# Kernel optimization log

Measured on AMD Instinct MI355X. Metric: run time of the kernel, lower is better.

The kernel has to match this reference:

```python
import jax, jax.numpy as jnp
import numpy as np

# Dimensions: S=Scount nodes, R=Rcount(=n_classes), B=len(source_index)
S, R, IN_F, OUT_F, H, B, C = 10000, 16, 128, 128, 4, 2048, 16
NEG = -9e15


def _bn(x, g, b):
    # BatchNorm1d, training-mode batch statistics (biased var), eps=1e-5
    m = x.mean(0)
    v = x.var(0)
    return (x - m) / jnp.sqrt(v + 1e-5) * g + b


def setup_inputs() -> dict:
    key = jax.random.key(0)
    ks = jax.random.split(key, 13)
    n = lambda k, s: jax.random.normal(k, s, jnp.float32) * 0.1
    return {
        "inter_adj": jax.random.randint(ks[0], (S, R), 0, 2, jnp.int32),
        "city_adj": jax.random.randint(ks[1], (S, S), 0, 2, jnp.int32),
        "province_adj": jax.random.randint(ks[2], (S, S), 0, 2, jnp.int32),
        "source_index": jax.random.randint(ks[3], (B,), 0, S, jnp.int32),
        "Sfeat": n(ks[4], (S, IN_F)),
        "Rfeat": n(ks[5], (R, IN_F)),
        "W1": n(ks[6], (H, IN_F, OUT_F)),
        "W2": n(ks[7], (H, IN_F, OUT_F)),
        "a": n(ks[8], (H, 2 * OUT_F)),
        "a3": n(ks[9], (H, 2 * OUT_F)),
        "a4": n(ks[10], (H, 2 * OUT_F)),
        "bn1_g": jnp.ones((H, OUT_F), jnp.float32),
        "bn1_b": jnp.zeros((H, OUT_F), jnp.float32),
        "bn2_g": jnp.ones((H, OUT_F), jnp.float32),
        "bn2_b": jnp.zeros((H, OUT_F), jnp.float32),
        "outW": n(ks[11], (H * R, C)),
        "outA": n(ks[12], (2 * C,)),
    }


def _forward(inter_adj, city_adj, province_adj, src, Sfeat, Rfeat,
             W1, W2, a, a3, a4, bn1_g, bn1_b, bn2_g, bn2_b, outW, outA):
    Fd = OUT_F
    inter_m = inter_adj > 0            # [S, R]
    city_m = city_adj[src] > 0         # [B, S]
    prov_m = province_adj[src] > 0     # [B, S]
    # Dropout is identity (eval mode); the concat+matmul attention scores are
    # computed as separable rank-1 terms instead of materializing O(S*R*2F).

    def head(W1h, W2h, ah, a3h, a4h, g1h, b1h, g2h, b2h):
        h1 = Rfeat @ W1h               # [R, F]
        h2 = Sfeat @ W2h               # [S, F]
        h2s = h2[src]                  # [B, F]
        # e12[i,j] = lrelu(a[:F].h1[j] + a[F:].h2[i])
        e12 = jax.nn.leaky_relu((h2 @ ah[Fd:])[:, None] + (h1 @ ah[:Fd])[None, :], 0.2)
        att_i = jax.nn.softmax(jnp.where(inter_m, e12, NEG), axis=1)   # [S, R]
        # cat([h3, h3]) -> score constant over the neighbor axis
        e3 = jax.nn.leaky_relu(h2s @ (a3h[:Fd] + a3h[Fd:]), 0.2)[:, None]  # [B,1]
        att3 = jax.nn.softmax(jnp.where(city_m, e3, NEG), axis=1)      # [B, S]
        e4 = jax.nn.leaky_relu(h2s @ (a4h[:Fd] + a4h[Fd:]), 0.2)[:, None]
        att4 = jax.nn.softmax(jnp.where(prov_m, e4, NEG), axis=1)
        InterRC = att_i @ h1                        # [S, F]
        IntraNC = (att3 + att4).T @ h2s             # [S, F]
        v = jax.nn.leaky_relu(_bn(att_i.T @ h2, g1h, b1h), 0.2)  # [R, F]
        u = jax.nn.leaky_relu(_bn(InterRC + IntraNC, g2h, b2h), 0.2)  # [S, F]
        return jax.nn.elu(u @ v.T)                  # [S, R]

    hx = jax.vmap(head)(W1, W2, a, a3, a4, bn1_g, bn1_b, bn2_g, bn2_b)  # [H,S,R]
    x = jnp.transpose(hx, (1, 0, 2)).reshape(S, H * R)
    # output GraphAttentionLayer
    h = x @ outW                                    # [S, C]
    e = jax.nn.leaky_relu(h @ (outA[:C] + outA[C:]), 0.2)[:, None]  # [S,1]
    att = jax.nn.softmax(jnp.where(inter_m, jnp.broadcast_to(e, inter_m.shape), NEG), axis=1)
    # elu inside layer, then elu again in ablation2, then log_softmax
    return jax.nn.log_softmax(jax.nn.elu(jax.nn.elu(att * h)), axis=1)


def reference(inter_adj, city_adj, province_adj, source_index, Sfeat, Rfeat,
              W1, W2, a, a3, a4, bn1_g, bn1_b, bn2_g, bn2_b, outW, outA):
    return _forward(inter_adj, city_adj, province_adj, source_index, Sfeat, Rfeat,
                    W1, W2, a, a3, a4, bn1_g, bn1_b, bn2_g, bn2_b, outW, outA)
```

## Files before the change

### kernel.cpp

```cpp
#include <hip/hip_runtime.h>
#include <hip/hip_bf16.h>
#include <stdint.h>

#define S_N 10000
#define MPAD 10112
#define B_N 2048
#define F_N 128

typedef __bf16 bf16x8 __attribute__((ext_vector_type(8)));
typedef __bf16 bf16x4 __attribute__((ext_vector_type(4)));
typedef float  f32x4  __attribute__((ext_vector_type(4)));
typedef unsigned long long u64;
typedef unsigned int u32;
typedef unsigned short u16;

union Bh8 { __bf16 h[8]; bf16x8 v; };

__device__ __forceinline__ float lrelu02(float x) { return x >= 0.0f ? x : 0.2f * x; }
__device__ __forceinline__ float eluf(float x)    { return x > 0.0f ? x : expm1f(x); }

__global__ __launch_bounds__(256) void k_bits_pre(const int* __restrict__ adj_c,
        const int* __restrict__ adj_p, const int* __restrict__ src,
        const float* __restrict__ Sfeat, const float* __restrict__ Rfeat,
        const float* __restrict__ W1, const float* __restrict__ W2, const float* __restrict__ a,
        u64* __restrict__ tcity, u64* __restrict__ tprov,
        u32* __restrict__ cc, u32* __restrict__ pc,
        __bf16* __restrict__ SfB, __bf16* __restrict__ W2T, __bf16* __restrict__ h1T,
        float* __restrict__ q) {
    const int bid = blockIdx.x, t = threadIdx.x;
    if (bid < 1280) {
        const int sc = bid % 20, wb = (bid / 20) % 32, mat = bid / 640;
        const int l = t & 63, w = t >> 6;
        const int* adj = mat ? adj_p : adj_c;
        u64* tb = mat ? tprov : tcity;
        u32* cnt = mat ? pc : cc;
        __shared__ u64 wt[64][8];
        __shared__ u32 lc[64];
        if (t < 64) lc[t] = 0;
        __syncthreads();
        const int s1 = sc * 512 + t;
        const int s2 = s1 + 256;
        for (int bb = 0; bb < 64; ++bb) {
            int row = src[wb * 64 + bb];
            const int* rp = adj + (size_t)row * S_N;
            int v1 = (s1 < S_N) ? rp[s1] : 0;
            int v2 = (s2 < S_N) ? rp[s2] : 0;
            u64 b1 = __ballot(v1 > 0);
            u64 b2 = __ballot(v2 > 0);
            if (l == 0) {
                wt[bb][w] = b1;
                wt[bb][w + 4] = b2;
                atomicAdd(&lc[bb], (u32)(__popcll(b1) + __popcll(b2)));
            }
        }
        __syncthreads();
        if (t < 64) atomicAdd(&cnt[wb * 64 + t], lc[t]);
        for (int tile = w; tile < 8; tile += 4) {
            u64 wv = wt[l][tile];
            u64 myw = 0;
            #pragma unroll
            for (int j = 0; j < 64; ++j) {
                u64 bal = __ballot((int)((wv >> j) & 1ull));
                if (l == j) myw = bal;
            }
            int s = sc * 512 + tile * 64 + l;
            if (s < MPAD) tb[(size_t)wb * MPAD + s] = myw;
        }
    } else if (bid < 6336) {
        int i = (bid - 1280) * 256 + t;
        int s = i >> 7;
        SfB[i] = (__bf16)(s < S_N ? Sfeat[i] : 0.0f);
    } else if (bid < 6592) {
        int idx = (bid - 6336) * 256 + t;
        int hn = idx >> 7, k = idx & 127;
        int h = hn >> 7, n = hn & 127;
        W2T[idx] = (__bf16)W2[(h * F_N + k) * F_N + n];
    } else {
        __shared__ float red[256];
        int b2i = bid - 6592;
        int h = b2i >> 4, r = b2i & 15;
        float hv = 0.0f;
        if (t < 128) {
            const float* rf = Rfeat + r * F_N;
            const float* wp = W1 + h * F_N * F_N + t;
            for (int k = 0; k < F_N; ++k) hv += rf[k] * wp[k * F_N];
        }
        red[t] = (t < 128) ? hv * a[h * 256 + t] : 0.0f;
        __syncthreads();
        for (int off = 128; off > 0; off >>= 1) {
            if (t < off) red[t] += red[t + off];
            __syncthreads();
        }
        if (t == 0) q[h * 16 + r] = red[0];
        if (t < 128) {
            h1T[(h * F_N + t) * 32 + r] = (__bf16)hv;
            h1T[(h * F_N + t) * 32 + 16 + r] = (__bf16)0.0f;
        }
    }
}

__global__ __launch_bounds__(256) void k_yz(const float* __restrict__ Sfeat,
        const int* __restrict__ src, const u32* __restrict__ cc, const u32* __restrict__ pc,
        __bf16* __restrict__ YT, __bf16* __restrict__ ZT) {
    int idx = blockIdx.x * 256 + threadIdx.x;
    int f = idx >> 11, b = idx & 2047;
    float sv = Sfeat[src[b] * F_N + f];
    float icc = cc[b] ? 1.0f / (float)cc[b] : 0.0f;
    float ipc = pc[b] ? 1.0f / (float)pc[b] : 0.0f;
    YT[f * B_N + b] = (__bf16)(sv * icc);
    ZT[f * B_N + b] = (__bf16)(sv * ipc);
}

__global__ __launch_bounds__(256) void g_T(const __bf16* __restrict__ YT, const __bf16* __restrict__ ZT,
        const u64* __restrict__ tcity, const u64* __restrict__ tprov,
        float* __restrict__ Tp, u32* __restrict__ tick, __bf16* __restrict__ Tb) {
    const int t = threadIdx.x, l = t & 63, w = t >> 6;
    const int wm = w >> 1, wn = w & 1;
    const int quad = l >> 4, ln = l & 15;
    const int s_blk = blockIdx.x * 128;
    const unsigned char* cb = (const unsigned char*)tcity;
    const unsigned char* pb = (const unsigned char*)tprov;
    __shared__ __align__(16) __bf16 lut[256][8];
    __shared__ u32 lastv;
    {
        #pragma unroll
        for (int j = 0; j < 8; ++j)
            lut[t][j] = ((t >> j) & 1) ? (__bf16)1.0f : (__bf16)0.0f;
    }
    __syncthreads();
    const f32x4 fz = {0.0f, 0.0f, 0.0f, 0.0f};
    f32x4 acc[4][4];
    #pragma unroll
    for (int mt = 0; mt < 4; ++mt)
        #pragma unroll
        for (int nt = 0; nt < 4; ++nt) acc[mt][nt] = fz;
    const int k_base = blockIdx.y * 512;
    for (int it = 0; it < 16; ++it) {
        int kk = k_base + it * 32;
        bf16x8 Ya[4], Za[4];
        #pragma unroll
        for (int mt = 0; mt < 4; ++mt) {
            int f = wm * 64 + mt * 16 + ln;
            Ya[mt] = *(const bf16x8*)(YT + f * B_N + kk + quad * 8);
            Za[mt] = *(const bf16x8*)(ZT + f * B_N + kk + quad * 8);
        }
        bf16x8 Bc[4], Bp[4];
        #pragma unroll
        for (int nt = 0; nt < 4; ++nt) {
            int s = s_blk + wn * 64 + nt * 16 + ln;
            size_t base = ((size_t)(kk >> 6) * MPAD + s) * 8 + ((kk >> 3) & 7) + quad;
            unsigned int cby = cb[base], pby = pb[base];
            Bc[nt] = *(const bf16x8*)(&lut[cby][0]);
            Bp[nt] = *(const bf16x8*)(&lut[pby][0]);
        }
        #pragma unroll
        for (int mt = 0; mt < 4; ++mt)
            #pragma unroll
            for (int nt = 0; nt < 4; ++nt) {
                acc[mt][nt] = __builtin_amdgcn_mfma_f32_16x16x32_bf16(Ya[mt], Bc[nt], acc[mt][nt], 0, 0, 0);
                acc[mt][nt] = __builtin_amdgcn_mfma_f32_16x16x32_bf16(Za[mt], Bp[nt], acc[mt][nt], 0, 0, 0);
            }
    }
    float* tp = Tp + (size_t)blockIdx.y * ((size_t)MPAD * F_N);
    #pragma unroll
    for (int nt = 0; nt < 4; ++nt) {
        int s = s_blk + wn * 64 + nt * 16 + ln;
        #pragma unroll
        for (int mt = 0; mt < 4; ++mt) {
            int f0 = wm * 64 + mt * 16 + quad * 4;
            *(f32x4*)(tp + (size_t)s * F_N + f0) = acc[mt][nt];
        }
    }
    __syncthreads();
    if (t == 0) {
        __threadfence();
        lastv = atomicAdd(&tick[blockIdx.x], 1u);
    }
    __syncthreads();
    if (lastv == 3u) {
        __threadfence();
        const size_t stride = (size_t)MPAD * F_N;
        for (int idx = t; idx < 4096; idx += 256) {
            size_t off = (size_t)s_blk * F_N + (size_t)idx * 4;
            f32x4 v0 = *(const f32x4*)(Tp + off);
            f32x4 v1 = *(const f32x4*)(Tp + stride + off);
            f32x4 v2 = *(const f32x4*)(Tp + 2 * stride + off);
            f32x4 v3 = *(const f32x4*)(Tp + 3 * stride + off);
            f32x4 sum = v0 + v1 + v2 + v3;
            bf16x4 o;
            #pragma unroll
            for (int j = 0; j < 4; ++j) o[j] = (__bf16)sum[j];
            *(bf16x4*)(Tb + off) = o;
        }
    }
}

__global__ __launch_bounds__(256) void g_h2attM(const __bf16* __restrict__ A, const __bf16* __restrict__ W2T,
        const float* __restrict__ a, const float* __restrict__ q, const int* __restrict__ inter,
        __bf16* __restrict__ attb, float* __restrict__ Mg) {
    const int t = threadIdx.x, l = t & 63, w = t >> 6;
    const int wm = w >> 1, wn = w & 1, quad = l >> 4, ln = l & 15;
    const int s0 = blockIdx.x * 128, h = blockIdx.y;
    __shared__ __bf16 h2T[128 * 136];
    __shared__ __bf16 attT[16 * 136];
    __shared__ float ps[128];
    if (t < 128) ps[t] = 0.0f;
    __syncthreads();
    const f32x4 fz = {0.0f, 0.0f, 0.0f, 0.0f};
    f32x4 acc[4][4];
    #pragma unroll
    for (int mt = 0; mt < 4; ++mt)
        #pragma unroll
        for (int nt = 0; nt < 4; ++nt) acc[mt][nt] = fz;
    #pragma unroll
    for (int it = 0; it < 4; ++it) {
        int kk = it * 32;
        bf16x8 af[4], bfr[4];
        #pragma unroll
        for (int mt = 0; mt < 4; ++mt)
            af[mt] = *(const bf16x8*)(A + (size_t)(s0 + wm * 64 + mt * 16 + ln) * F_N + kk + quad * 8);
        #pragma unroll
        for (int nt = 0; nt < 4; ++nt)
            bfr[nt] = *(const bf16x8*)(W2T + (size_t)(h * F_N + wn * 64 + nt * 16 + ln) * F_N + kk + quad * 8);
        #pragma unroll
        for (int mt = 0; mt < 4; ++mt)
            #pragma unroll
            for (int nt = 0; nt < 4; ++nt)
                acc[mt][nt] = __builtin_amdgcn_mfma_f32_16x16x32_bf16(af[mt], bfr[nt], acc[mt][nt], 0, 0, 0);
    }
    float a2v[4];
    #pragma unroll
    for (int nt = 0; nt < 4; ++nt) a2v[nt] = a[h * 256 + 128 + wn * 64 + nt * 16 + ln];
    #pragma unroll
    for (int mt = 0; mt < 4; ++mt) {
        #pragma unroll
        for (int nt = 0; nt < 4; ++nt) {
            bf16x4 o;
            #pragma unroll
            for (int j = 0; j < 4; ++j) o[j] = (__bf16)acc[mt][nt][j];
            *(bf16x4*)(&h2T[(wn * 64 + nt * 16 + ln) * 136 + wm * 64 + mt * 16 + quad * 4]) = o;
        }
        #pragma unroll
        for (int r = 0; r < 4; ++r) {
            float pp = 0.0f;
            #pragma unroll
            for (int nt = 0; nt < 4; ++nt) pp += acc[mt][nt][r] * a2v[nt];
            #pragma unroll
            for (int m = 8; m > 0; m >>= 1) pp += __shfl_xor(pp, m, 16);
            if (ln == 0) atomicAdd(&ps[wm * 64 + mt * 16 + quad * 4 + r], pp);
        }
    }
    __syncthreads();
    if (t < 128) {
        int s = s0 + t;
        if (s < S_N) {
            float pv = ps[t];
            float e[16];
            int msk[16], cn = 0;
            float mx = -3e38f;
            #pragma unroll
            for (int c = 0; c < 16; ++c) {
                msk[c] = inter[s * 16 + c] > 0;
                cn += msk[c];
                e[c] = lrelu02(pv + q[h * 16 + c]);
                if (msk[c]) mx = fmaxf(mx, e[c]);
            }
            float sm = 0.0f;
            #pragma unroll
            for (int c = 0; c < 16; ++c) {
                e[c] = msk[c] ? expf(e[c] - mx) : 0.0f;
                sm += e[c];
            }
            float inv = cn > 0 ? 1.0f / sm : 0.0f;
            #pragma unroll
            for (int c = 0; c < 16; ++c) {
                float av = cn > 0 ? e[c] * inv : 0.0625f;
                attb[((size_t)h * MPAD + s) * 16 + c] = (__bf16)av;
                attT[c * 136 + t] = (__bf16)av;
            }
        } else {
            #pragma unroll
            for (int c = 0; c < 16; ++c) {
                attb[((size_t)h * MPAD + s) * 16 + c] = (__bf16)0.0f;
                attT[c * 136 + t] = (__bf16)0.0f;
            }
        }
    }
    __syncthreads();
    #pragma unroll
    for (int fi = 0; fi < 2; ++fi) {
        int ft = 2 * w + fi;
        f32x4 macc = fz;
        #pragma unroll
        for (int kit = 0; kit < 4; ++kit) {
            bf16x8 av = *(const bf16x8*)(&attT[ln * 136 + kit * 32 + quad * 8]);
            bf16x8 bv = *(const bf16x8*)(&h2T[(ft * 16 + ln) * 136 + kit * 32 + quad * 8]);
            macc = __builtin_amdgcn_mfma_f32_16x16x32_bf16(av, bv, macc, 0, 0, 0);
        }
        #pragma unroll
        for (int r = 0; r < 4; ++r)
            atomicAdd(&Mg[(h * 16 + quad * 4 + r) * F_N + ft * 16 + ln], macc[r]);
    }
}

__global__ __launch_bounds__(256) void g_P(const __bf16* __restrict__ Tb, const __bf16* __restrict__ W2T,
        const __bf16* __restrict__ attb, const __bf16* __restrict__ h1T,
        __bf16* __restrict__ P, float* __restrict__ usum, float* __restrict__ usq) {
    const int t = threadIdx.x, l = t & 63, w = t >> 6;
    const int wm = w >> 1, wn = w & 1, quad = l >> 4, ln = l & 15;
    const int s0 = blockIdx.x * 128, h = blockIdx.y;
    __shared__ __bf16 sP[128 * 136];
    __shared__ float lsum[128], lsq[128];
    if (t < 128) { lsum[t] = 0.0f; lsq[t] = 0.0f; }
    __syncthreads();
    const f32x4 fz = {0.0f, 0.0f, 0.0f, 0.0f};
    f32x4 acc[4][4];
    #pragma unroll
    for (int mt = 0; mt < 4; ++mt)
        #pragma unroll
        for (int nt = 0; nt < 4; ++nt) acc[mt][nt] = fz;
    {
        bf16x8 a2[4], b2[4];
        #pragma unroll
        for (int mt = 0; mt < 4; ++mt) {
            int s = s0 + wm * 64 + mt * 16 + ln;
            Bh8 az;
            az.v = *(const bf16x8*)(attb + ((size_t)h * MPAD + s) * 16 + (quad & 1) * 8);
            if (quad >= 2) {
                #pragma unroll
                for (int j = 0; j < 8; ++j) az.h[j] = (__bf16)0.0f;
            }
            a2[mt] = az.v;
        }
        #pragma unroll
        for (int nt = 0; nt < 4; ++nt) {
            int f = wn * 64 + nt * 16 + ln;
            b2[nt] = *(const bf16x8*)(h1T + ((size_t)(h * F_N + f)) * 32 + quad * 8);
        }
        #pragma unroll
        for (int mt = 0; mt < 4; ++mt)
            #pragma unroll
            for (int nt = 0; nt < 4; ++nt)
                acc[mt][nt] = __builtin_amdgcn_mfma_f32_16x16x32_bf16(a2[mt], b2[nt], acc[mt][nt], 0, 0, 0);
    }
    #pragma unroll
    for (int it = 0; it < 4; ++it) {
        int kk = it * 32;
        bf16x8 af[4], bfr[4];
        #pragma unroll
        for (int mt = 0; mt < 4; ++mt)
            af[mt] = *(const bf16x8*)(Tb + (size_t)(s0 + wm * 64 + mt * 16 + ln) * F_N + kk + quad * 8);
        #pragma unroll
        for (int nt = 0; nt < 4; ++nt)
            bfr[nt] = *(const bf16x8*)(W2T + (size_t)(h * F_N + wn * 64 + nt * 16 + ln) * F_N + kk + quad * 8);
        #pragma unroll
        for (int mt = 0; mt < 4; ++mt)
            #pragma unroll
            for (int nt = 0; nt < 4; ++nt)
                acc[mt][nt] = __builtin_amdgcn_mfma_f32_16x16x32_bf16(af[mt], bfr[nt], acc[mt][nt], 0, 0, 0);
    }
    #pragma unroll
    for (int nt = 0; nt < 4; ++nt) {
        int f = wn * 64 + nt * 16 + ln;
        float p1 = 0.0f, p2 = 0.0f;
        #pragma unroll
        for (int mt = 0; mt < 4; ++mt) {
            int sb = wm * 64 + mt * 16 + quad * 4;
            #pragma unroll
            for (int r = 0; r < 4; ++r) {
                float val = acc[mt][nt][r];
                sP[(sb + r) * 136 + f] = (__bf16)val;
                p1 += val; p2 += val * val;
            }
        }
        atomicAdd(&lsum[f], p1);
        atomicAdd(&lsq[f], p2);
    }
    __syncthreads();
    if (t < 128) {
        atomicAdd(&usum[h * F_N + t], lsum[t]);
        atomicAdd(&usq[h * F_N + t], lsq[t]);
    }
    for (int g = t; g < 2048; g += 256) {
        int sl = g >> 4, fg = (g & 15) * 8;
        bf16x8 v = *(const bf16x8*)(&sP[sl * 136 + fg]);
        *(bf16x8*)(P + ((size_t)h * MPAD + s0 + sl) * F_N + fg) = v;
    }
}

__global__ __launch_bounds__(256) void g_out(const __bf16* __restrict__ P,
        const float* __restrict__ usum, const float* __restrict__ usq, const float* __restrict__ Mg,
        const float* __restrict__ g1, const float* __restrict__ b1,
        const float* __restrict__ g2, const float* __restrict__ b2,
        const float* __restrict__ outW, const int* __restrict__ inter, float* __restrict__ out) {
    const int t = threadIdx.x, l = t & 63, w = t >> 6, quad = l >> 4, ln = l & 15;
    const int s0 = blockIdx.x * 32;
    __shared__ __bf16 v_lds[64 * 136];
    __shared__ float G_lds[32 * 68];
    __shared__ float scs[512], shs[512];
    __shared__ float W_lds[1024];
    for (int i = t; i < 1024; i += 256) W_lds[i] = outW[i];
    if (t < 128) {
        #pragma unroll
        for (int h = 0; h < 4; ++h) {
            int i = h * F_N + t;
            float mean = usum[i] * (1.0f / S_N);
            float var = usq[i] * (1.0f / S_N) - mean * mean;
            float sc = g2[i] * rsqrtf(var + 1e-5f);
            scs[i] = sc;
            shs[i] = b2[i] - mean * sc;
        }
    }
    {
        int f = t & 127;
        int hb = (t >> 7) * 2;
        #pragma unroll
        for (int hh = hb; hh < hb + 2; ++hh) {
            float mv[16], sa = 0.0f, sb = 0.0f;
            #pragma unroll
            for (int r = 0; r < 16; ++r) {
                mv[r] = Mg[(hh * 16 + r) * F_N + f];
                sa += mv[r]; sb += mv[r] * mv[r];
            }
            float m1 = sa * 0.0625f, v1 = sb * 0.0625f - m1 * m1;
            int i = hh * F_N + f;
            float g = g1[i] * rsqrtf(v1 + 1e-5f);
            float bb = b1[i] - m1 * g;
            #pragma unroll
            for (int r = 0; r < 16; ++r)
                v_lds[(hh * 16 + r) * 136 + f] = (__bf16)lrelu02(mv[r] * g + bb);
        }
    }
    __syncthreads();
    const int h = w;
    const f32x4 fz = {0.0f, 0.0f, 0.0f, 0.0f};
    #pragma unroll
    for (int mt = 0; mt < 2; ++mt) {
        f32x4 gacc = fz;
        int s = s0 + mt * 16 + ln;
        #pragma unroll
        for (int kit = 0; kit < 4; ++kit) {
            int k0 = kit * 32 + quad * 8;
            bf16x8 pv = *(const bf16x8*)(P + ((size_t)h * MPAD + s) * F_N + k0);
            Bh8 af;
            #pragma unroll
            for (int j = 0; j < 8; ++j) {
                int f = k0 + j;
                af.h[j] = (__bf16)lrelu02((float)pv[j] * scs[h * F_N + f] + shs[h * F_N + f]);
            }
            bf16x8 bv = *(const bf16x8*)(&v_lds[(h * 16 + ln) * 136 + k0]);
            gacc = __builtin_amdgcn_mfma_f32_16x16x32_bf16(af.v, bv, gacc, 0, 0, 0);
        }
        #pragma unroll
        for (int r = 0; r < 4; ++r)
            G_lds[(mt * 16 + quad * 4 + r) * 68 + h * 16 + ln] = eluf(gacc[r]);
    }
    __syncthreads();
    const int c = t & 15, ss = t >> 4;
    #pragma unroll
    for (int pass = 0; pass < 2; ++pass) {
        int sl = pass * 16 + ss;
        int s = s0 + sl;
        float hm = 0.0f;
        #pragma unroll
        for (int j = 0; j < 64; ++j) hm += G_lds[sl * 68 + j] * W_lds[j * 16 + c];
        int valid = s < S_N;
        int msk = valid ? (inter[(valid ? s : 0) * 16 + c] > 0) : 0;
        int cn = msk;
        #pragma unroll
        for (int m = 8; m > 0; m >>= 1) cn += __shfl_xor(cn, m, 16);
        float attf = cn > 0 ? (msk ? 1.0f / (float)cn : 0.0f) : 0.0625f;
        float y = eluf(eluf(attf * hm));
        float mx = y;
        #pragma unroll
        for (int m = 8; m > 0; m >>= 1) mx = fmaxf(mx, __shfl_xor(mx, m, 16));
        float ex = expf(y - mx);
        float sm = ex;
        #pragma unroll
        for (int m = 8; m > 0; m >>= 1) sm += __shfl_xor(sm, m, 16);
        if (valid) out[s * 16 + c] = y - mx - logf(sm);
    }
}

extern "C" void kernel_launch(void* const* d_in, const int* in_sizes, int n_in,
                              void* d_out, int out_size, void* d_ws, size_t ws_size,
                              hipStream_t stream) {
    const int* inter = (const int*)d_in[0];
    const int* city  = (const int*)d_in[1];
    const int* prov  = (const int*)d_in[2];
    const int* src   = (const int*)d_in[3];
    const float* Sfeat = (const float*)d_in[4];
    const float* Rfeat = (const float*)d_in[5];
    const float* W1 = (const float*)d_in[6];
    const float* W2 = (const float*)d_in[7];
    const float* a  = (const float*)d_in[8];
    const float* g1 = (const float*)d_in[11];
    const float* b1 = (const float*)d_in[12];
    const float* g2 = (const float*)d_in[13];
    const float* b2 = (const float*)d_in[14];
    const float* outW = (const float*)d_in[15];
    float* out = (float*)d_out;

    char* p = (char*)d_ws;
    float* M    = (float*)p; p += 4 * 16 * F_N * 4;
    float* usum = (float*)p; p += 2048;
    float* usq  = (float*)p; p += 2048;
    u32*   cc   = (u32*)p;   p += 8192;
    u32*   pc   = (u32*)p;   p += 8192;
    u32*   tick = (u32*)p;   p += 512;
    size_t zbytes = (size_t)(p - (char*)d_ws);
    u64* tcity = (u64*)p; p += 32 * (size_t)MPAD * 8;
    u64* tprov = (u64*)p; p += 32 * (size_t)MPAD * 8;
    __bf16* YT  = (__bf16*)p; p += (size_t)F_N * B_N * 2;
    __bf16* ZT  = (__bf16*)p; p += (size_t)F_N * B_N * 2;
    __bf16* SfB = (__bf16*)p; p += (size_t)MPAD * F_N * 2;
    __bf16* W2T = (__bf16*)p; p += 512 * 128 * 2;
    __bf16* h1T = (__bf16*)p; p += 4 * 128 * 32 * 2;
    float*  q   = (float*)p;  p += 512;
    float*  Tp  = (float*)p;  p += 4 * (size_t)MPAD * F_N * 4;
    __bf16* Tb  = (__bf16*)p; p += (size_t)MPAD * F_N * 2;
    __bf16* attb= (__bf16*)p; p += 4 * (size_t)MPAD * 16 * 2;
    __bf16* P   = (__bf16*)p; p += 4 * (size_t)MPAD * F_N * 2;

    hipMemsetAsync(d_ws, 0, zbytes, stream);
    k_bits_pre<<<6656, 256, 0, stream>>>(city, prov, src, Sfeat, Rfeat, W1, W2, a,
                                         tcity, tprov, cc, pc, SfB, W2T, h1T, q);
    k_yz      <<<1024, 256, 0, stream>>>(Sfeat, src, cc, pc, YT, ZT);
    g_T       <<<dim3(79, 4), 256, 0, stream>>>(YT, ZT, tcity, tprov, Tp, tick, Tb);
    g_h2attM  <<<dim3(79, 4), 256, 0, stream>>>(SfB, W2T, a, q, inter, attb, M);
    g_P       <<<dim3(79, 4), 256, 0, stream>>>(Tb, W2T, attb, h1T, P, usum, usq);
    g_out     <<<316, 256, 0, stream>>>(P, usum, usq, M, g1, b1, g2, b2, outW, inter, out);
}
```

Baseline: 803.4 us.

## Build transposed adjacency bitmasks per thread and expand bits to bf16 in registers

The bitmask pre-pass now has each thread load two adjacent int columns per source row and build its 64-bit column mask directly in registers. This replaces the shared-memory staging and the 64-step ballot transpose. In the T GEMM kernel, the LDS lookup table that expanded mask bytes to bf16 vectors is replaced by computing the bf16 bit patterns with ALU ops in registers. Together these remove LDS traffic, a barrier and the transpose work, at the cost of more VALU instructions per MFMA tile and strided 8-byte global loads.

```diff
diff --git a/kernel.cpp b/kernel.cpp
--- a/kernel.cpp
+++ b/kernel.cpp
@@ -14,6 +14,7 @@
 typedef unsigned int u32;
 typedef unsigned short u16;
 
+union Bf8 { u16 us[8]; bf16x8 v; };
 union Bh8 { __bf16 h[8]; bf16x8 v; };
 
 __device__ __forceinline__ float lrelu02(float x) { return x >= 0.0f ? x : 0.2f * x; }
@@ -30,41 +31,37 @@
     const int bid = blockIdx.x, t = threadIdx.x;
     if (bid < 1280) {
         const int sc = bid % 20, wb = (bid / 20) % 32, mat = bid / 640;
-        const int l = t & 63, w = t >> 6;
+        const int l = t & 63;
         const int* adj = mat ? adj_p : adj_c;
         u64* tb = mat ? tprov : tcity;
         u32* cnt = mat ? pc : cc;
-        __shared__ u64 wt[64][8];
         __shared__ u32 lc[64];
         if (t < 64) lc[t] = 0;
         __syncthreads();
-        const int s1 = sc * 512 + t;
-        const int s2 = s1 + 256;
+        const int s1 = sc * 512 + 2 * t;
+        const int in_rng = (s1 < S_N);
+        const int* base0 = adj + s1;
+        u64 w1 = 0, w2 = 0;
+        #pragma unroll 8
         for (int bb = 0; bb < 64; ++bb) {
             int row = src[wb * 64 + bb];
-            const int* rp = adj + (size_t)row * S_N;
-            int v1 = (s1 < S_N) ? rp[s1] : 0;
-            int v2 = (s2 < S_N) ? rp[s2] : 0;
-            u64 b1 = __ballot(v1 > 0);
-            u64 b2 = __ballot(v2 > 0);
-            if (l == 0) {
-                wt[bb][w] = b1;
-                wt[bb][w + 4] = b2;
-                atomicAdd(&lc[bb], (u32)(__popcll(b1) + __popcll(b2)));
-            }
+            int vx = 0, vy = 0;
+            if (in_rng) {
+                int2 v = *(const int2*)(base0 + (size_t)row * S_N);
+                vx = v.x; vy = v.y;
+            }
+            u64 b1 = __ballot(vx > 0);
+            u64 b2 = __ballot(vy > 0);
+            w1 |= (u64)(vx > 0 ? 1u : 0u) << bb;
+            w2 |= (u64)(vy > 0 ? 1u : 0u) << bb;
+            if (l == 0) atomicAdd(&lc[bb], (u32)(__popcll(b1) + __popcll(b2)));
         }
         __syncthreads();
         if (t < 64) atomicAdd(&cnt[wb * 64 + t], lc[t]);
-        for (int tile = w; tile < 8; tile += 4) {
-            u64 wv = wt[l][tile];
-            u64 myw = 0;
-            #pragma unroll
-            for (int j = 0; j < 64; ++j) {
-                u64 bal = __ballot((int)((wv >> j) & 1ull));
-                if (l == j) myw = bal;
-            }
-            int s = sc * 512 + tile * 64 + l;
-            if (s < MPAD) tb[(size_t)wb * MPAD + s] = myw;
+        if (s1 < MPAD) {
+            u64* dst = tb + (size_t)wb * MPAD + s1;
+            dst[0] = w1;
+            dst[1] = w2;
         }
     } else if (bid < 6336) {
         int i = (bid - 1280) * 256 + t;
@@ -120,14 +117,7 @@
     const int s_blk = blockIdx.x * 128;
     const unsigned char* cb = (const unsigned char*)tcity;
     const unsigned char* pb = (const unsigned char*)tprov;
-    __shared__ __align__(16) __bf16 lut[256][8];
     __shared__ u32 lastv;
-    {
-        #pragma unroll
-        for (int j = 0; j < 8; ++j)
-            lut[t][j] = ((t >> j) & 1) ? (__bf16)1.0f : (__bf16)0.0f;
-    }
-    __syncthreads();
     const f32x4 fz = {0.0f, 0.0f, 0.0f, 0.0f};
     f32x4 acc[4][4];
     #pragma unroll
@@ -150,8 +140,13 @@
             int s = s_blk + wn * 64 + nt * 16 + ln;
             size_t base = ((size_t)(kk >> 6) * MPAD + s) * 8 + ((kk >> 3) & 7) + quad;
             unsigned int cby = cb[base], pby = pb[base];
-            Bc[nt] = *(const bf16x8*)(&lut[cby][0]);
-            Bp[nt] = *(const bf16x8*)(&lut[pby][0]);
+            Bf8 uc, up;
+            #pragma unroll
+            for (int j = 0; j < 8; ++j) {
+                uc.us[j] = ((cby >> j) & 1u) ? (u16)0x3F80 : (u16)0;
+                up.us[j] = ((pby >> j) & 1u) ? (u16)0x3F80 : (u16)0;
+            }
+            Bc[nt] = uc.v; Bp[nt] = up.v;
         }
         #pragma unroll
         for (int mt = 0; mt < 4; ++mt)
```

Result: faster. 769.3 us (-4.2%).
